# Kernel optimization log

Measured on AMD Instinct MI355X. Metric: run time of the kernel, lower is better.

The kernel has to match this reference:

```python
import jax, jax.numpy as jnp
import numpy as np

K = 4  # spline order (degree K-1)


def bspline_basis(x, t, k):
    """Evaluate the k nonzero B-spline basis functions of order k at x.

    x: [B, I] floats; t: [G+2k-1] clamped knot vector.
    Returns (idx [B,I,k] int32 basis indices, basis [B,I,k] values),
    using the de Boor / NURBS-book triangular recursion (vectorized over B,I;
    Python loops only over the small fixed order k).
    """
    m = t.shape[0]
    # interval index: t[i] <= x < t[i+1], clamped to valid span [k-1, m-k-1]
    i = jnp.clip(jnp.searchsorted(t, x, side='right') - 1, k - 1, m - k - 1)
    p = k - 1
    N = [jnp.ones_like(x)]
    left, right = [], []
    for j in range(1, p + 1):
        left.append(x - t[i + 1 - j])
        right.append(t[i + j] - x)
        saved = jnp.zeros_like(x)
        Nn = []
        for r in range(j):
            temp = N[r] / (right[r] + left[j - 1 - r])
            Nn.append(saved + right[r] * temp)
            saved = left[j - 1 - r] * temp
        Nn.append(saved)
        N = Nn
    idx = jnp.stack([i - p + j for j in range(k)], axis=-1)   # [B,I,k]
    basis = jnp.stack(N, axis=-1)                             # [B,I,k]
    return idx, basis


def setup_inputs() -> dict:
    key = jax.random.key(0)
    k1, k2 = jax.random.split(key)
    B, I, O, G, k = 2048, 128, 128, 64, K
    t0, t1 = -1.0, 1.0
    x = jax.random.uniform(k1, (B, I), jnp.float32, minval=t0, maxval=t1)
    # xavier_normal_ for fan_in=in_dim, fan_out=out_dim (per-slice heuristic)
    std = (2.0 / (I + O)) ** 0.5
    w = jax.random.normal(k2, (G + k, I, O), jnp.float32) * std
    t = jnp.concatenate([
        jnp.full((k - 1,), t0, jnp.float32),
        jnp.linspace(t0, t1, G + 1, dtype=jnp.float32),
        jnp.full((k - 1,), t1, jnp.float32),
    ])
    return {"x": x, "w": w, "t": t}


def reference(x, w, t):
    k = K
    B, I = x.shape
    O = w.shape[2]
    idx, basis = bspline_basis(x, t, k)                       # [B,I,k]
    # activation slot uses the last row of w (torch index -1)
    act_idx = jnp.full((B, I, 1), w.shape[0] - 1, idx.dtype)
    idx_full = jnp.concatenate([idx, act_idx], axis=-1)       # [B,I,k+1]
    y = jnp.concatenate([basis, jax.nn.silu(x)[..., None]], axis=-1)  # [B,I,k+1]
    wt = jnp.transpose(w, (1, 0, 2))                          # [I, G+k, O]
    w2 = wt[jnp.arange(I)[None, :, None], idx_full]           # [B,I,k+1,O] gather
    return jnp.einsum('bij,bijo->bo', y, w2)                  # [B,O]
```

## Files before the change

### kernel.cpp

```cpp
#include <hip/hip_runtime.h>
#include <math.h>

#define B_TOTAL 2048
#define I_DIM   128
#define O_DIM   128
#define GK      68
#define NKNOT   71
#define W_ELEMS ((size_t)GK * I_DIM * O_DIM)
#define WS_MIN  (W_ELEMS * 2)
#define SLICE_DW (GK * O_DIM / 2)
#define ROW_DW   (O_DIM / 2)

__device__ __forceinline__ float rdlanef(float v, int sl) {
    return __int_as_float(__builtin_amdgcn_readlane(__float_as_int(v), sl));
}
__device__ __forceinline__ unsigned short f2bf(float f) {
    unsigned u = __float_as_uint(f);
    return (unsigned short)((u + 0x7fffu + ((u >> 16) & 1u)) >> 16);
}
__device__ __forceinline__ float bflo(unsigned u) { return __uint_as_float(u << 16); }
__device__ __forceinline__ float bfhi(unsigned u) { return __uint_as_float(u & 0xffff0000u); }

__device__ __forceinline__ void coef_eval(float xv, const float* t_sh,
                                          float& c0, float& c1, float& c2,
                                          float& c3, float& c4, int& g0) {
    int ik = 3 + (int)floorf((xv + 1.0f) * 32.0f);
    ik = min(max(ik, 3), 66);
    while (ik < 66 && xv >= t_sh[ik + 1]) ++ik;
    while (ik > 3 && xv < t_sh[ik]) --ik;
    float l0, l1, l2, r0, r1, r2;
    float N0 = 1.0f, N1, N2, N3;
    l0 = xv - t_sh[ik];  r0 = t_sh[ik + 1] - xv;
    { float temp = N0 / (r0 + l0); N0 = r0 * temp; N1 = l0 * temp; }
    l1 = xv - t_sh[ik - 1];  r1 = t_sh[ik + 2] - xv;
    { float saved = 0.0f, temp;
      temp = N0 / (r0 + l1); N0 = saved + r0 * temp; saved = l1 * temp;
      temp = N1 / (r1 + l0); N1 = saved + r1 * temp; N2 = l0 * temp; }
    l2 = xv - t_sh[ik - 2];  r2 = t_sh[ik + 3] - xv;
    { float saved = 0.0f, temp;
      temp = N0 / (r0 + l2); N0 = saved + r0 * temp; saved = l2 * temp;
      temp = N1 / (r1 + l1); N1 = saved + r1 * temp; saved = l1 * temp;
      temp = N2 / (r2 + l0); N2 = saved + r2 * temp; N3 = l0 * temp; }
    c0 = N0; c1 = N1; c2 = N2; c3 = N3;
    c4 = xv / (1.0f + expf(-xv));
    g0 = ik - 3;
}

__global__ __launch_bounds__(256)
void wcvt(const float* __restrict__ w, unsigned short* __restrict__ wbf) {
    const int tid = threadIdx.x;
    const int p   = blockIdx.x * 8 + (tid >> 5);
    const int oq  = (tid & 31) * 4;
    const int g   = p >> 7;
    const int i   = p & 127;
    const float4 v = *(const float4*)(w + (size_t)p * O_DIM + oq);
    ushort4 o4;
    o4.x = f2bf(v.x); o4.y = f2bf(v.y); o4.z = f2bf(v.z); o4.w = f2bf(v.w);
    *(ushort4*)(wbf + ((size_t)i * GK + g) * O_DIM + oq) = o4;
}

__global__ __launch_bounds__(512, 2)
void flashkan_sync(const float* __restrict__ x,
                   const unsigned short* __restrict__ wbf,
                   const float* __restrict__ t,
                   float* __restrict__ out) {
    __shared__ float t_sh[NKNOT];

    const int tid  = threadIdx.x;
    const int wave = tid >> 6;
    const int lane = tid & 63;
    const int b    = blockIdx.x * 8 + wave;

    if (tid < NKNOT) t_sh[tid] = t[tid];
    __syncthreads();

    float a0, a1, a2, a3, a4;  int ga;
    float b0, b1, b2, b3, b4;  int gb;
    coef_eval(x[(size_t)b * I_DIM + lane],      t_sh, a0, a1, a2, a3, a4, ga);
    coef_eval(x[(size_t)b * I_DIM + lane + 64], t_sh, b0, b1, b2, b3, b4, gb);

    const unsigned* wdw = (const unsigned*)wbf;
    float ax = 0.0f, ay = 0.0f;

    #pragma unroll 4
    for (int k = 0; k < 64; ++k) {
        const float c0 = rdlanef(a0, k), c1 = rdlanef(a1, k);
        const float c2 = rdlanef(a2, k), c3 = rdlanef(a3, k);
        const float c4 = rdlanef(a4, k);
        const int   g0 = __builtin_amdgcn_readlane(ga, k);

        const unsigned* rp = wdw + (size_t)k * SLICE_DW + g0 * ROW_DW + lane;
        const unsigned* sp = wdw + (size_t)k * SLICE_DW + 67 * ROW_DW + lane;
        const unsigned u0 = rp[0];
        const unsigned u1 = rp[ROW_DW];
        const unsigned u2 = rp[2 * ROW_DW];
        const unsigned u3 = rp[3 * ROW_DW];
        const unsigned u4 = *sp;

        ax += c0 * bflo(u0) + c1 * bflo(u1) + c2 * bflo(u2)
            + c3 * bflo(u3) + c4 * bflo(u4);
        ay += c0 * bfhi(u0) + c1 * bfhi(u1) + c2 * bfhi(u2)
            + c3 * bfhi(u3) + c4 * bfhi(u4);
    }

    #pragma unroll 4
    for (int k = 0; k < 64; ++k) {
        const float c0 = rdlanef(b0, k), c1 = rdlanef(b1, k);
        const float c2 = rdlanef(b2, k), c3 = rdlanef(b3, k);
        const float c4 = rdlanef(b4, k);
        const int   g0 = __builtin_amdgcn_readlane(gb, k);

        const unsigned* rp = wdw + (size_t)(k + 64) * SLICE_DW + g0 * ROW_DW + lane;
        const unsigned* sp = wdw + (size_t)(k + 64) * SLICE_DW + 67 * ROW_DW + lane;
        const unsigned u0 = rp[0];
        const unsigned u1 = rp[ROW_DW];
        const unsigned u2 = rp[2 * ROW_DW];
        const unsigned u3 = rp[3 * ROW_DW];
        const unsigned u4 = *sp;

        ax += c0 * bflo(u0) + c1 * bflo(u1) + c2 * bflo(u2)
            + c3 * bflo(u3) + c4 * bflo(u4);
        ay += c0 * bfhi(u0) + c1 * bfhi(u1) + c2 * bfhi(u2)
            + c3 * bfhi(u3) + c4 * bfhi(u4);
    }

    *(float2*)(out + (size_t)b * O_DIM + lane * 2) = make_float2(ax, ay);
}

__global__ __launch_bounds__(256)
void flashkan_gather_f32(const float* __restrict__ x,
                         const float* __restrict__ w,
                         const float* __restrict__ t,
                         float* __restrict__ out) {
    __shared__ float t_sh[NKNOT];
    __shared__ float psum[4][O_DIM];
    const int tid  = threadIdx.x;
    const int b    = blockIdx.x;
    const int wave = tid >> 6;
    const int lane = tid & 63;
    const int l32  = lane & 31;
    if (tid < NKNOT) t_sh[tid] = t[tid];
    __syncthreads();
    float cf0, cf1, cf2, cf3, cf4; int cg;
    coef_eval(x[(size_t)b * I_DIM + wave * 32 + l32], t_sh,
              cf0, cf1, cf2, cf3, cf4, cg);
    const int i_base = wave * 32;
    float ax = 0.0f, ay = 0.0f;
    #pragma unroll 8
    for (int k = 0; k < 32; ++k) {
        const float c0 = rdlanef(cf0, k), c1 = rdlanef(cf1, k);
        const float c2 = rdlanef(cf2, k), c3 = rdlanef(cf3, k);
        const float c4 = rdlanef(cf4, k);
        const int   g0 = __builtin_amdgcn_readlane(cg, k);
        const int i = i_base + k;
        const float2* base = (const float2*)(w + (size_t)i * O_DIM) + lane;
        const size_t rs = (size_t)I_DIM * O_DIM / 2;
        const float2 v0 = base[(size_t)g0 * rs];
        const float2 v1 = base[(size_t)(g0 + 1) * rs];
        const float2 v2 = base[(size_t)(g0 + 2) * rs];
        const float2 v3 = base[(size_t)(g0 + 3) * rs];
        const float2 v4 = base[(size_t)(GK - 1) * rs];
        ax += c0 * v0.x + c1 * v1.x + c2 * v2.x + c3 * v3.x + c4 * v4.x;
        ay += c0 * v0.y + c1 * v1.y + c2 * v2.y + c3 * v3.y + c4 * v4.y;
    }
    psum[wave][lane * 2]     = ax;
    psum[wave][lane * 2 + 1] = ay;
    __syncthreads();
    if (tid < O_DIM) {
        out[(size_t)b * O_DIM + tid] =
            psum[0][tid] + psum[1][tid] + psum[2][tid] + psum[3][tid];
    }
}

extern "C" void kernel_launch(void* const* d_in, const int* in_sizes, int n_in,
                              void* d_out, int out_size, void* d_ws, size_t ws_size,
                              hipStream_t stream) {
    const float* x = (const float*)d_in[0];
    const float* w = (const float*)d_in[1];
    const float* t = (const float*)d_in[2];
    float* out = (float*)d_out;

    if (ws_size >= WS_MIN) {
        unsigned short* wbf = (unsigned short*)d_ws;
        wcvt<<<(int)(W_ELEMS / (8 * 128)), 256, 0, stream>>>(w, wbf);
        flashkan_sync<<<B_TOTAL / 8, 512, 0, stream>>>(x, wbf, t, out);
    } else {
        flashkan_gather_f32<<<B_TOTAL, 256, 0, stream>>>(x, w, t, out);
    }
}
```

Before: 32.19 us.

## Split each wave into quads so one wide load covers all four spline rows

The four 16-lane groups of each wave now each own one of the four consecutive spline rows. This works because those rows are contiguous 256-byte runs in the bf16 weight layout, so a single 16-byte load per lane fetches all four instead of four separate dword loads. Spline coefficients are staged in a per-wave LDS table, with the silu coefficient pre-scaled by 1/4. That table replaces the many per-iteration readlanes. Partial sums are then reduced across the groups with xor shuffles. In exchange the silu row is read redundantly by every group, and the kernel needs more LDS and accumulator registers.

```diff
diff --git a/kernel.cpp b/kernel.cpp
--- a/kernel.cpp
+++ b/kernel.cpp
@@ -8,8 +8,7 @@
 #define NKNOT   71
 #define W_ELEMS ((size_t)GK * I_DIM * O_DIM)
 #define WS_MIN  (W_ELEMS * 2)
-#define SLICE_DW (GK * O_DIM / 2)
-#define ROW_DW   (O_DIM / 2)
+#define SLICE_B (GK * O_DIM * 2)
 
 __device__ __forceinline__ float rdlanef(float v, int sl) {
     return __int_as_float(__builtin_amdgcn_readlane(__float_as_int(v), sl));
@@ -60,71 +59,88 @@
 }
 
 __global__ __launch_bounds__(512, 2)
-void flashkan_sync(const float* __restrict__ x,
+void flashkan_quad(const float* __restrict__ x,
                    const unsigned short* __restrict__ wbf,
                    const float* __restrict__ t,
                    float* __restrict__ out) {
     __shared__ float t_sh[NKNOT];
+    __shared__ float tab[8][I_DIM][8];
 
     const int tid  = threadIdx.x;
     const int wave = tid >> 6;
-    const int lane = tid & 63;
+    const int l    = tid & 63;
     const int b    = blockIdx.x * 8 + wave;
+    const int q2   = (l >> 4) * 2;
 
     if (tid < NKNOT) t_sh[tid] = t[tid];
     __syncthreads();
 
     float a0, a1, a2, a3, a4;  int ga;
-    float b0, b1, b2, b3, b4;  int gb;
-    coef_eval(x[(size_t)b * I_DIM + lane],      t_sh, a0, a1, a2, a3, a4, ga);
-    coef_eval(x[(size_t)b * I_DIM + lane + 64], t_sh, b0, b1, b2, b3, b4, gb);
-
-    const unsigned* wdw = (const unsigned*)wbf;
-    float ax = 0.0f, ay = 0.0f;
+    float e0, e1, e2, e3, e4;  int gb;
+    coef_eval(x[(size_t)b * I_DIM + l],      t_sh, a0, a1, a2, a3, a4, ga);
+    coef_eval(x[(size_t)b * I_DIM + l + 64], t_sh, e0, e1, e2, e3, e4, gb);
+
+    {
+        const float a4q = a4 * 0.25f, e4q = e4 * 0.25f;
+        float4* tp0 = (float4*)&tab[wave][l][0];
+        tp0[0] = make_float4(a0, a4q, a1, a4q);
+        tp0[1] = make_float4(a2, a4q, a3, a4q);
+        float4* tp1 = (float4*)&tab[wave][l + 64][0];
+        tp1[0] = make_float4(e0, e4q, e1, e4q);
+        tp1[1] = make_float4(e2, e4q, e3, e4q);
+    }
+
+    const char* wb = (const char*)wbf;
+    const int spl_off  = l * 16;
+    const int silu_off = 67 * 256 + (l & 15) * 16;
+
+    float acc[8];
+    #pragma unroll
+    for (int e = 0; e < 8; ++e) acc[e] = 0.0f;
 
     #pragma unroll 4
     for (int k = 0; k < 64; ++k) {
-        const float c0 = rdlanef(a0, k), c1 = rdlanef(a1, k);
-        const float c2 = rdlanef(a2, k), c3 = rdlanef(a3, k);
-        const float c4 = rdlanef(a4, k);
-        const int   g0 = __builtin_amdgcn_readlane(ga, k);
-
-        const unsigned* rp = wdw + (size_t)k * SLICE_DW + g0 * ROW_DW + lane;
-        const unsigned* sp = wdw + (size_t)k * SLICE_DW + 67 * ROW_DW + lane;
-        const unsigned u0 = rp[0];
-        const unsigned u1 = rp[ROW_DW];
-        const unsigned u2 = rp[2 * ROW_DW];
-        const unsigned u3 = rp[3 * ROW_DW];
-        const unsigned u4 = *sp;
-
-        ax += c0 * bflo(u0) + c1 * bflo(u1) + c2 * bflo(u2)
-            + c3 * bflo(u3) + c4 * bflo(u4);
-        ay += c0 * bfhi(u0) + c1 * bfhi(u1) + c2 * bfhi(u2)
-            + c3 * bfhi(u3) + c4 * bfhi(u4);
-    }
-
+        const int g0 = __builtin_amdgcn_readlane(ga, k);
+        const float2 cq = *(const float2*)&tab[wave][k][q2];
+        const char* sl = wb + (size_t)k * SLICE_B;
+        const uint4 u = *(const uint4*)(sl + g0 * 256 + spl_off);
+        const uint4 s = *(const uint4*)(sl + silu_off);
+        acc[0] += cq.x * bflo(u.x) + cq.y * bflo(s.x);
+        acc[1] += cq.x * bfhi(u.x) + cq.y * bfhi(s.x);
+        acc[2] += cq.x * bflo(u.y) + cq.y * bflo(s.y);
+        acc[3] += cq.x * bfhi(u.y) + cq.y * bfhi(s.y);
+        acc[4] += cq.x * bflo(u.z) + cq.y * bflo(s.z);
+        acc[5] += cq.x * bfhi(u.z) + cq.y * bfhi(s.z);
+        acc[6] += cq.x * bflo(u.w) + cq.y * bflo(s.w);
+        acc[7] += cq.x * bfhi(u.w) + cq.y * bfhi(s.w);
+    }
     #pragma unroll 4
     for (int k = 0; k < 64; ++k) {
-        const float c0 = rdlanef(b0, k), c1 = rdlanef(b1, k);
-        const float c2 = rdlanef(b2, k), c3 = rdlanef(b3, k);
-        const float c4 = rdlanef(b4, k);
-        const int   g0 = __builtin_amdgcn_readlane(gb, k);
-
-        const unsigned* rp = wdw + (size_t)(k + 64) * SLICE_DW + g0 * ROW_DW + lane;
-        const unsigned* sp = wdw + (size_t)(k + 64) * SLICE_DW + 67 * ROW_DW + lane;
-        const unsigned u0 = rp[0];
-        const unsigned u1 = rp[ROW_DW];
-        const unsigned u2 = rp[2 * ROW_DW];
-        const unsigned u3 = rp[3 * ROW_DW];
-        const unsigned u4 = *sp;
-
-        ax += c0 * bflo(u0) + c1 * bflo(u1) + c2 * bflo(u2)
-            + c3 * bflo(u3) + c4 * bflo(u4);
-        ay += c0 * bfhi(u0) + c1 * bfhi(u1) + c2 * bfhi(u2)
-            + c3 * bfhi(u3) + c4 * bfhi(u4);
-    }
-
-    *(float2*)(out + (size_t)b * O_DIM + lane * 2) = make_float2(ax, ay);
+        const int g0 = __builtin_amdgcn_readlane(gb, k);
+        const float2 cq = *(const float2*)&tab[wave][k + 64][q2];
+        const char* sl = wb + (size_t)(k + 64) * SLICE_B;
+        const uint4 u = *(const uint4*)(sl + g0 * 256 + spl_off);
+        const uint4 s = *(const uint4*)(sl + silu_off);
+        acc[0] += cq.x * bflo(u.x) + cq.y * bflo(s.x);
+        acc[1] += cq.x * bfhi(u.x) + cq.y * bfhi(s.x);
+        acc[2] += cq.x * bflo(u.y) + cq.y * bflo(s.y);
+        acc[3] += cq.x * bfhi(u.y) + cq.y * bfhi(s.y);
+        acc[4] += cq.x * bflo(u.z) + cq.y * bflo(s.z);
+        acc[5] += cq.x * bfhi(u.z) + cq.y * bfhi(s.z);
+        acc[6] += cq.x * bflo(u.w) + cq.y * bflo(s.w);
+        acc[7] += cq.x * bfhi(u.w) + cq.y * bfhi(s.w);
+    }
+
+    #pragma unroll
+    for (int e = 0; e < 8; ++e) acc[e] += __shfl_xor(acc[e], 16);
+    #pragma unroll
+    for (int e = 0; e < 8; ++e) acc[e] += __shfl_xor(acc[e], 32);
+
+    if (l < 16) {
+        float* dp = out + (size_t)b * O_DIM + l * 8;
+        *(float4*)dp       = make_float4(acc[0], acc[1], acc[2], acc[3]);
+        *(float4*)(dp + 4) = make_float4(acc[4], acc[5], acc[6], acc[7]);
+    }
 }
 
 __global__ __launch_bounds__(256)
@@ -183,7 +199,7 @@
     if (ws_size >= WS_MIN) {
         unsigned short* wbf = (unsigned short*)d_ws;
         wcvt<<<(int)(W_ELEMS / (8 * 128)), 256, 0, stream>>>(w, wbf);
-        flashkan_sync<<<B_TOTAL / 8, 512, 0, stream>>>(x, wbf, t, out);
+        flashkan_quad<<<B_TOTAL / 8, 512, 0, stream>>>(x, wbf, t, out);
     } else {
         flashkan_gather_f32<<<B_TOTAL, 256, 0, stream>>>(x, w, t, out);
     }
```

Result: slower. 53.82 us (+67.2%).

## Split each batch row across four waves with half-wave basis-pair loads

Applied to the files above, without the earlier changes.

Replaces the one-wave-per-batch-row kernel, which looped over all 128 inputs, with one 256-thread block per row. Each wave handles 32 inputs, partial sums are reduced through shared memory, and the launch bound now requests higher occupancy. Inside a wave, the two half-waves each load 8-byte chunks from two of the four basis rows, and a cross-half shuffle combines them. This shortens each wave's serial dependency chain and issues fewer, wider loads, at the cost of more blocks and an extra shared-memory reduction with a block barrier.

```diff
diff --git a/kernel.cpp b/kernel.cpp
--- a/kernel.cpp
+++ b/kernel.cpp
@@ -8,8 +8,7 @@
 #define NKNOT   71
 #define W_ELEMS ((size_t)GK * I_DIM * O_DIM)
 #define WS_MIN  (W_ELEMS * 2)
-#define SLICE_DW (GK * O_DIM / 2)
-#define ROW_DW   (O_DIM / 2)
+#define SLICE_B (GK * O_DIM * 2)
 
 __device__ __forceinline__ float rdlanef(float v, int sl) {
     return __int_as_float(__builtin_amdgcn_readlane(__float_as_int(v), sl));
@@ -59,72 +58,70 @@
     *(ushort4*)(wbf + ((size_t)i * GK + g) * O_DIM + oq) = o4;
 }
 
-__global__ __launch_bounds__(512, 2)
-void flashkan_sync(const float* __restrict__ x,
-                   const unsigned short* __restrict__ wbf,
-                   const float* __restrict__ t,
-                   float* __restrict__ out) {
+__global__ __launch_bounds__(256, 8)
+void flashkan_gather(const float* __restrict__ x,
+                     const unsigned short* __restrict__ wbf,
+                     const float* __restrict__ t,
+                     float* __restrict__ out) {
     __shared__ float t_sh[NKNOT];
+    __shared__ float psum[4][O_DIM];
 
     const int tid  = threadIdx.x;
+    const int b    = blockIdx.x;
     const int wave = tid >> 6;
     const int lane = tid & 63;
-    const int b    = blockIdx.x * 8 + wave;
+    const int h    = lane >> 5;
+    const int l32  = lane & 31;
 
     if (tid < NKNOT) t_sh[tid] = t[tid];
     __syncthreads();
 
-    float a0, a1, a2, a3, a4;  int ga;
-    float b0, b1, b2, b3, b4;  int gb;
-    coef_eval(x[(size_t)b * I_DIM + lane],      t_sh, a0, a1, a2, a3, a4, ga);
-    coef_eval(x[(size_t)b * I_DIM + lane + 64], t_sh, b0, b1, b2, b3, b4, gb);
+    float cf0, cf1, cf2, cf3, cf4;
+    int   cg;
+    coef_eval(x[(size_t)b * I_DIM + wave * 32 + l32], t_sh,
+              cf0, cf1, cf2, cf3, cf4, cg);
 
-    const unsigned* wdw = (const unsigned*)wbf;
-    float ax = 0.0f, ay = 0.0f;
+    const char* wb = (const char*)wbf + (size_t)(wave * 32) * SLICE_B;
+    const int lo8 = l32 * 8;
 
-    #pragma unroll 4
-    for (int k = 0; k < 64; ++k) {
-        const float c0 = rdlanef(a0, k), c1 = rdlanef(a1, k);
-        const float c2 = rdlanef(a2, k), c3 = rdlanef(a3, k);
-        const float c4 = rdlanef(a4, k);
-        const int   g0 = __builtin_amdgcn_readlane(ga, k);
+    float a0 = 0.0f, a1 = 0.0f, a2 = 0.0f, a3 = 0.0f;
 
-        const unsigned* rp = wdw + (size_t)k * SLICE_DW + g0 * ROW_DW + lane;
-        const unsigned* sp = wdw + (size_t)k * SLICE_DW + 67 * ROW_DW + lane;
-        const unsigned u0 = rp[0];
-        const unsigned u1 = rp[ROW_DW];
-        const unsigned u2 = rp[2 * ROW_DW];
-        const unsigned u3 = rp[3 * ROW_DW];
-        const unsigned u4 = *sp;
+    #pragma unroll
+    for (int k = 0; k < 32; ++k) {
+        const float c0 = rdlanef(cf0, k), c1 = rdlanef(cf1, k);
+        const float c2 = rdlanef(cf2, k), c3 = rdlanef(cf3, k);
+        const float c4 = rdlanef(cf4, k);
+        const int   g0 = __builtin_amdgcn_readlane(cg, k);
 
-        ax += c0 * bflo(u0) + c1 * bflo(u1) + c2 * bflo(u2)
-            + c3 * bflo(u3) + c4 * bflo(u4);
-        ay += c0 * bfhi(u0) + c1 * bfhi(u1) + c2 * bfhi(u2)
-            + c3 * bfhi(u3) + c4 * bfhi(u4);
+        const float cA  = h ? c1 : c0;
+        const float cB  = h ? c3 : c2;
+        const float c4h = h ? 0.0f : c4;
+
+        const char* sl = wb + (size_t)k * SLICE_B;
+        const uint2 uA = *(const uint2*)(sl + (g0 + h) * 256 + lo8);
+        const uint2 uB = *(const uint2*)(sl + (g0 + 2 + h) * 256 + lo8);
+        const uint2 su = *(const uint2*)(sl + 67 * 256 + lo8);
+
+        a0 += cA * bflo(uA.x) + cB * bflo(uB.x) + c4h * bflo(su.x);
+        a1 += cA * bfhi(uA.x) + cB * bfhi(uB.x) + c4h * bfhi(su.x);
+        a2 += cA * bflo(uA.y) + cB * bflo(uB.y) + c4h * bflo(su.y);
+        a3 += cA * bfhi(uA.y) + cB * bfhi(uB.y) + c4h * bfhi(su.y);
     }
 
-    #pragma unroll 4
-    for (int k = 0; k < 64; ++k) {
-        const float c0 = rdlanef(b0, k), c1 = rdlanef(b1, k);
-        const float c2 = rdlanef(b2, k), c3 = rdlanef(b3, k);
-        const float c4 = rdlanef(b4, k);
-        const int   g0 = __builtin_amdgcn_readlane(gb, k);
+    a0 += __shfl_xor(a0, 32);
+    a1 += __shfl_xor(a1, 32);
+    a2 += __shfl_xor(a2, 32);
+    a3 += __shfl_xor(a3, 32);
 
-        const unsigned* rp = wdw + (size_t)(k + 64) * SLICE_DW + g0 * ROW_DW + lane;
-        const unsigned* sp = wdw + (size_t)(k + 64) * SLICE_DW + 67 * ROW_DW + lane;
-        const unsigned u0 = rp[0];
-        const unsigned u1 = rp[ROW_DW];
-        const unsigned u2 = rp[2 * ROW_DW];
-        const unsigned u3 = rp[3 * ROW_DW];
-        const unsigned u4 = *sp;
+    if (lane < 32) {
+        *(float4*)&psum[wave][l32 * 4] = make_float4(a0, a1, a2, a3);
+    }
+    __syncthreads();
 
-        ax += c0 * bflo(u0) + c1 * bflo(u1) + c2 * bflo(u2)
-            + c3 * bflo(u3) + c4 * bflo(u4);
-        ay += c0 * bfhi(u0) + c1 * bfhi(u1) + c2 * bfhi(u2)
-            + c3 * bfhi(u3) + c4 * bfhi(u4);
+    if (tid < O_DIM) {
+        out[(size_t)b * O_DIM + tid] =
+            psum[0][tid] + psum[1][tid] + psum[2][tid] + psum[3][tid];
     }
-
-    *(float2*)(out + (size_t)b * O_DIM + lane * 2) = make_float2(ax, ay);
 }
 
 __global__ __launch_bounds__(256)
@@ -183,7 +180,7 @@
     if (ws_size >= WS_MIN) {
         unsigned short* wbf = (unsigned short*)d_ws;
         wcvt<<<(int)(W_ELEMS / (8 * 128)), 256, 0, stream>>>(w, wbf);
-        flashkan_sync<<<B_TOTAL / 8, 512, 0, stream>>>(x, wbf, t, out);
+        flashkan_gather<<<B_TOTAL, 256, 0, stream>>>(x, wbf, t, out);
     } else {
         flashkan_gather_f32<<<B_TOTAL, 256, 0, stream>>>(x, w, t, out);
     }
```

Measured after the change: 64.53 us. +100.5%, slower.
